# Kernel tuning notes

Hardware: AMD Instinct MI355X
Metric: run time of the kernel (lower is better)

The kernel has to match this reference:

```python
import jax, jax.numpy as jnp
import numpy as np

N_FFT = 2048
HOP = 441
DIM = 512


def _hann(n_fft):
    # torch.hann_window (periodic): 0.5*(1 - cos(2*pi*n/N))
    n = jnp.arange(n_fft, dtype=jnp.float32)
    return 0.5 * (1.0 - jnp.cos(2.0 * jnp.pi * n / n_fft))


def setup_inputs() -> dict:
    key = jax.random.key(0)
    k1, k2, k3 = jax.random.split(key, 3)
    x = jax.random.normal(k1, (4, 2, 1323000), dtype=jnp.float32)
    W_enc = 1e-4 * jax.random.normal(k2, (DIM, N_FFT), dtype=jnp.float32)
    W_dec = 1e-4 * jax.random.normal(k3, (N_FFT, DIM), dtype=jnp.float32)
    return {"x": x, "W_enc": W_enc, "W_dec": W_dec, "length": 1323000}


def reference(x, W_enc, W_dec, length):
    b, c, L = x.shape
    pad = N_FFT // 2
    window = _hann(N_FFT)

    # ---- encode ----
    xp = jnp.pad(x, ((0, 0), (0, 0), (pad, pad)), mode="reflect")  # (b,c,L+n_fft)
    Lp = xp.shape[-1]
    t = (Lp - N_FFT) // HOP + 1  # num frames
    idx = jnp.arange(t)[:, None] * HOP + jnp.arange(N_FFT)[None, :]  # (t, n)
    frames = xp[..., idx] * window  # (b,c,t,n) -- the overlapping unfold buffer
    feat = jnp.einsum("bctn,mn->bctm", frames, W_enc)  # (b,c,t,dim)

    # ---- decode ----
    rec = jnp.einsum("bctm,nm->bctn", feat, W_dec)  # (b,c,t,n)
    L2 = N_FFT + (t - 1) * HOP
    # overlap-add (F.fold) over merged (b*c) rows
    out = jnp.zeros((b * c, L2), dtype=rec.dtype)
    out = out.at[:, idx].add(rec.reshape(b * c, t, N_FFT))
    # window normalization (second fold in the original)
    win_norm = jnp.zeros((L2,), dtype=rec.dtype)
    win_norm = win_norm.at[idx].add(jnp.broadcast_to(window, (t, N_FFT)))
    out = out / jnp.clip(win_norm, 1e-8)
    out = out.reshape(b, c, L2)[..., pad:pad + length]
    return out
```

## Files before the change

### kernel.cpp

```cpp
#include <hip/hip_runtime.h>
#include <stdint.h>

typedef unsigned short u16;
typedef unsigned int u32;
typedef __attribute__((ext_vector_type(8))) short short8;
typedef __attribute__((ext_vector_type(4))) float f32x4;

#define L_IN   1323000
#define PAD    1024
#define HOP    441
#define T_FR   3001
#define M_ROWS 24008
#define NB     3008
#define RPAD   448
#define K1E    2240
#define K2     2560
#define W_2PI_N 3.0679615757712823e-3f

__device__ __forceinline__ u16 f2bf(float f) {
  union { float f; u32 u; } v; v.f = f;
  u32 r = v.u + 0x7FFFu + ((v.u >> 16) & 1u);
  return (u16)(r >> 16);
}

__device__ __forceinline__ void gload16(const void* g, void* l) {
  __builtin_amdgcn_global_load_lds(
      (const __attribute__((address_space(1))) u32*)g,
      (__attribute__((address_space(3))) u32*)l, 16, 0, 0);
}

__device__ __forceinline__ void tile_from_bid(int bid, int& m0, int& n0) {
  int g = (bid & 7) * 94 + (bid >> 3);
  m0 = (g >> 2) * 128;
  n0 = (g & 3) * 128;
}

__global__ void prep_all(const float* __restrict__ x,
                         const float* __restrict__ W_enc, const float* __restrict__ W_dec,
                         u16* __restrict__ xb, u16* __restrict__ wh2,
                         u16* __restrict__ b2, float* __restrict__ zeros) {
  int stride = gridDim.x * blockDim.x;
  int tid0 = blockIdx.x * blockDim.x + threadIdx.x;
  for (int idx = tid0; idx < 64; idx += stride) zeros[idx] = 0.f;
  for (int idx = tid0; idx < 8 * NB * RPAD; idx += stride) {
    int bc = idx / (NB * RPAD);
    int rem = idx - bc * (NB * RPAD);
    int u = rem / RPAD;
    int r = rem - u * RPAD;
    int s = HOP * u + r - PAD;
    int ja = s < 0 ? -s : s;
    int jb = 2 * L_IN - 2 - ja;
    int jr = ja < jb ? ja : jb;
    xb[idx] = f2bf(x[(size_t)bc * L_IN + jr]);
  }
  for (int idx = tid0; idx < 512 * K1E; idx += stride) {
    int m = idx / K1E;
    int k = idx - m * K1E;
    int j = k / RPAD;
    int r = k - j * RPAD;
    int n = HOP * j + r;
    float v = 0.f;
    if (r < HOP && n < 2048)
      v = (0.5f - 0.5f * cosf(W_2PI_N * (float)n)) * W_enc[m * 2048 + n];
    wh2[idx] = f2bf(v);
  }
  for (int idx = tid0; idx < 512 * K2; idx += stride) {
    int r = idx / K2;
    int k = idx - r * K2;
    int j = k >> 9;
    int m = k & 511;
    int n = HOP * j + r;
    float v = 0.f;
    if (r < HOP && n < 2048) {
      float s = 0.f;
      #pragma unroll
      for (int jj = 0; jj < 5; ++jj) {
        int nn = HOP * jj + r;
        if (nn < 2048) s += 0.5f - 0.5f * cosf(W_2PI_N * (float)nn);
      }
      v = W_dec[n * 512 + m] / fmaxf(s, 1e-8f);
    }
    b2[idx] = f2bf(v);
  }
}

__device__ __forceinline__ void mfma_tile(const u16* sA, const u16* sB, f32x4 acc[4][4],
                                          int lane, int wr, int wc) {
  const int lr = lane & 15;
  const int hi = lane >> 4;
  #pragma unroll
  for (int ks = 0; ks < 2; ++ks) {
    const int off = (((ks * 4 + hi) ^ (lr & 7)) << 3);
    short8 af[4], bg[4];
    #pragma unroll
    for (int f = 0; f < 4; ++f)
      af[f] = *(const short8*)(sA + (wr + f * 16 + lr) * 64 + off);
    #pragma unroll
    for (int f = 0; f < 4; ++f)
      bg[f] = *(const short8*)(sB + (wc + f * 16 + lr) * 64 + off);
    #pragma unroll
    for (int mf = 0; mf < 4; ++mf)
      #pragma unroll
      for (int nf = 0; nf < 4; ++nf)
        acc[mf][nf] = __builtin_amdgcn_mfma_f32_16x16x32_bf16(af[mf], bg[nf], acc[mf][nf], 0, 0, 0);
  }
}


__global__ __launch_bounds__(256, 2)
void gemm_enc(const u16* __restrict__ xb, const u16* __restrict__ wh2,
              u16* __restrict__ featb) {
  __shared__ u16 sA[128 * 64];
  __shared__ u16 sB[128 * 64];
  const int tid = threadIdx.x;
  const int lane = tid & 63;
  const int w = tid >> 6;
  int m0, n0;
  tile_from_bid(blockIdx.x, m0, n0);
  const int colsw = (((lane & 7) ^ ((lane >> 3) & 7)) << 3);

  const u16* bsrc[4];
  const u16* asrc[4];
  #pragma unroll
  for (int i = 0; i < 4; ++i) {
    int row = (i * 4 + w) * 8 + (lane >> 3);
    bsrc[i] = wh2 + (size_t)(n0 + row) * K1E + colsw;
    int rg = m0 + row;
    int rgc = rg < M_ROWS ? rg : (M_ROWS - 1);
    int bc = rgc / T_FR;
    int t  = rgc - bc * T_FR;
    asrc[i] = xb + ((size_t)bc * NB + t) * RPAD + colsw;
  }

  f32x4 acc[4][4];
  #pragma unroll
  for (int a = 0; a < 4; ++a)
    #pragma unroll
    for (int b = 0; b < 4; ++b) acc[a][b] = f32x4{0.f, 0.f, 0.f, 0.f};

  const int wr = (w >> 1) * 64, wc = (w & 1) * 64;

  for (int kc = 0; kc < K1E; kc += 64) {
    __syncthreads();
    #pragma unroll
    for (int i = 0; i < 4; ++i)
      gload16(bsrc[i] + kc, &sB[(i * 4 + w) * 512]);
    #pragma unroll
    for (int i = 0; i < 4; ++i)
      gload16(asrc[i] + kc, &sA[(i * 4 + w) * 512]);
    __syncthreads();
    mfma_tile(sA, sB, acc, lane, wr, wc);
  }

  #pragma unroll
  for (int mf = 0; mf < 4; ++mf) {
    #pragma unroll
    for (int e = 0; e < 4; ++e) {
      int rg = m0 + wr + mf * 16 + ((lane >> 4) << 2) + e;
      if (rg < M_ROWS) {
        #pragma unroll
        for (int nf = 0; nf < 4; ++nf) {
          int cg = n0 + wc + nf * 16 + (lane & 15);
          featb[(size_t)rg * 512 + cg] = f2bf(acc[mf][nf][e]);
        }
      }
    }
  }
}


__global__ __launch_bounds__(256, 2)
void gemm_dec(const u16* __restrict__ featb, const u16* __restrict__ b2,
              const u16* __restrict__ zeros, float* __restrict__ out) {
  __shared__ u16 sA[128 * 64];
  __shared__ u16 sB[128 * 64];
  const int tid = threadIdx.x;
  const int lane = tid & 63;
  const int w = tid >> 6;
  const int m0 = blockIdx.x * 128;
  const int n0 = blockIdx.y * 128;
  const int colsw = (((lane & 7) ^ ((lane >> 3) & 7)) << 3);

  const u16* bsrc[4];
  const u16* fsrc[4];
  int qiv[4];
  unsigned vmask = 0;
  #pragma unroll
  for (int i = 0; i < 4; ++i) {
    int row = (i * 4 + w) * 8 + (lane >> 3);
    bsrc[i] = b2 + (size_t)(n0 + row) * K2 + colsw;
    int rg = m0 + row;
    int rgc = rg < M_ROWS ? rg : (M_ROWS - 1);
    int bc = rgc / T_FR;
    int qi = rgc - bc * T_FR;
    if (rg < M_ROWS) vmask |= 1u << i;
    qiv[i] = qi;
    fsrc[i] = featb + (size_t)(bc * T_FR + qi + 2) * 512 + colsw;
  }

  f32x4 acc[4][4];
  #pragma unroll
  for (int a = 0; a < 4; ++a)
    #pragma unroll
    for (int b = 0; b < 4; ++b) acc[a][b] = f32x4{0.f, 0.f, 0.f, 0.f};

  const int wr = (w >> 1) * 64, wc = (w & 1) * 64;

  for (int kc = 0; kc < K2; kc += 64) {
    int jt = kc >> 9;
    __syncthreads();
    #pragma unroll
    for (int i = 0; i < 4; ++i)
      gload16(bsrc[i] + kc, &sB[(i * 4 + w) * 512]);
    #pragma unroll
    for (int i = 0; i < 4; ++i) {
      int t = qiv[i] + 2 - jt;
      bool ok = ((vmask >> i) & 1) && (t >= 0) && (t <= 3000);
      const u16* pa = ok ? (fsrc[i] + kc - 1024 * jt) : (zeros + colsw);
      gload16(pa, &sA[(i * 4 + w) * 512]);
    }
    __syncthreads();
    mfma_tile(sA, sB, acc, lane, wr, wc);
  }

  const int lr16 = lane & 15;
  #pragma unroll
  for (int mf = 0; mf < 4; ++mf) {
    #pragma unroll
    for (int e = 0; e < 4; ++e) {
      int rg = m0 + wr + mf * 16 + ((lane >> 4) << 2) + e;
      if (rg < M_ROWS) {
        int bc = rg / T_FR;
        int qi = rg - bc * T_FR;
        int ib = HOP * qi - 142;
        bool interior = (qi >= 2) && (qi <= 2998);
        #pragma unroll
        for (int nf = 0; nf < 4; ++nf) {
          int cg = n0 + wc + nf * 16 + lr16;
          if (cg < HOP) {
            int oi = ib + cg;
            if (oi >= 0 && oi < L_IN) {
              float v = acc[mf][nf][e];
              if (!interior) {
                float sf = 0.f, se = 0.f;
                #pragma unroll
                for (int j = 0; j < 5; ++j) {
                  int n = HOP * j + cg;
                  float h = (n < 2048) ? (0.5f - 0.5f * cosf(W_2PI_N * (float)n)) : 0.f;
                  sf += h;
                  if ((unsigned)(qi + 2 - j) <= 3000u) se += h;
                }
                v *= fmaxf(sf, 1e-8f) / fmaxf(se, 1e-8f);
              }
              out[(size_t)bc * L_IN + oi] = v;
            }
          }
        }
      }
    }
  }
}


extern "C" void kernel_launch(void* const* d_in, const int* in_sizes, int n_in,
                              void* d_out, int out_size, void* d_ws, size_t ws_size,
                              hipStream_t stream) {
  const float* x     = (const float*)d_in[0];
  const float* W_enc = (const float*)d_in[1];
  const float* W_dec = (const float*)d_in[2];
  float* out = (float*)d_out;
  char* ws = (char*)d_ws;

  u16* xb = (u16*)d_out;

  u16*   wh2   = (u16*)  (ws + 0);
  u16*   b2    = (u16*)  (ws + 2293760);
  u16*   featb = (u16*)  (ws + 4915200);
  float* zeros = (float*)(ws + 29499392);

  prep_all<<<2048, 256, 0, stream>>>(x, W_enc, W_dec, xb, wh2, b2, zeros);
  gemm_enc<<<752, 256, 0, stream>>>(xb, wh2, featb);
  gemm_dec<<<dim3(188, 4), 256, 0, stream>>>(featb, b2, (const u16*)zeros, out);
}
```

Baseline: 156.5 us.

## Precompose encoder and decoder weights into one convolution-like GEMM with edge fixup

Since encode and decode are both linear, the change composes W_dec and W_enc (with window and normalization folded in) into a single weight of shape 512x4032 over padded input samples. The main GEMM then maps raw framed input directly to output and no longer materializes the intermediate features. Edge frames, where the normalization differs, are handled by a tiny encoder GEMM, a dot-product kernel and a scatter. The main GEMM's K dimension grows from 2240+2560 to 4032 and the weight precomposition adds work. Composing the weights in bf16 and rounding the result back to bf16 changes numerical error.

```diff
diff --git a/kernel.cpp b/kernel.cpp
--- a/kernel.cpp
+++ b/kernel.cpp
@@ -11,10 +11,10 @@
 #define HOP    441
 #define T_FR   3001
 #define M_ROWS 24008
-#define NB     3008
+#define NBE    3016
 #define RPAD   448
 #define K1E    2240
-#define K2     2560
+#define KC     4032
 #define W_2PI_N 3.0679615757712823e-3f
 
 __device__ __forceinline__ u16 f2bf(float f) {
@@ -22,36 +22,36 @@
   u32 r = v.u + 0x7FFFu + ((v.u >> 16) & 1u);
   return (u16)(r >> 16);
 }
-
+__device__ __forceinline__ float bf2f(u16 s) {
+  union { u32 u; float f; } v; v.u = ((u32)s) << 16;
+  return v.f;
+}
 __device__ __forceinline__ void gload16(const void* g, void* l) {
   __builtin_amdgcn_global_load_lds(
       (const __attribute__((address_space(1))) u32*)g,
       (__attribute__((address_space(3))) u32*)l, 16, 0, 0);
 }
 
-__device__ __forceinline__ void tile_from_bid(int bid, int& m0, int& n0) {
-  int g = (bid & 7) * 94 + (bid >> 3);
-  m0 = (g >> 2) * 128;
-  n0 = (g & 3) * 128;
-}
-
 __global__ void prep_all(const float* __restrict__ x,
                          const float* __restrict__ W_enc, const float* __restrict__ W_dec,
-                         u16* __restrict__ xb, u16* __restrict__ wh2,
-                         u16* __restrict__ b2, float* __restrict__ zeros) {
+                         u16* __restrict__ xbe, u16* __restrict__ wh2,
+                         u16* __restrict__ wh2t, u16* __restrict__ b2) {
   int stride = gridDim.x * blockDim.x;
   int tid0 = blockIdx.x * blockDim.x + threadIdx.x;
-  for (int idx = tid0; idx < 64; idx += stride) zeros[idx] = 0.f;
-  for (int idx = tid0; idx < 8 * NB * RPAD; idx += stride) {
-    int bc = idx / (NB * RPAD);
-    int rem = idx - bc * (NB * RPAD);
+  for (int idx = tid0; idx < 8 * NBE * RPAD; idx += stride) {
+    int bc = idx / (NBE * RPAD);
+    int rem = idx - bc * (NBE * RPAD);
     int u = rem / RPAD;
     int r = rem - u * RPAD;
-    int s = HOP * u + r - PAD;
-    int ja = s < 0 ? -s : s;
-    int jb = 2 * L_IN - 2 - ja;
-    int jr = ja < jb ? ja : jb;
-    xb[idx] = f2bf(x[(size_t)bc * L_IN + jr]);
+    u16 v = 0;
+    if (u >= 4 && u <= 3008) {
+      int s = HOP * (u - 4) + r - PAD;
+      int ja = s < 0 ? -s : s;
+      int jb = 2 * L_IN - 2 - ja;
+      int jr = ja < jb ? ja : jb;
+      v = f2bf(x[(size_t)bc * L_IN + jr]);
+    }
+    xbe[idx] = v;
   }
   for (int idx = tid0; idx < 512 * K1E; idx += stride) {
     int m = idx / K1E;
@@ -62,11 +62,13 @@
     float v = 0.f;
     if (r < HOP && n < 2048)
       v = (0.5f - 0.5f * cosf(W_2PI_N * (float)n)) * W_enc[m * 2048 + n];
-    wh2[idx] = f2bf(v);
-  }
-  for (int idx = tid0; idx < 512 * K2; idx += stride) {
-    int r = idx / K2;
-    int k = idx - r * K2;
+    u16 b = f2bf(v);
+    wh2[idx] = b;
+    wh2t[k * 512 + m] = b;
+  }
+  for (int idx = tid0; idx < 512 * 2560; idx += stride) {
+    int r = idx / 2560;
+    int k = idx - r * 2560;
     int j = k >> 9;
     int m = k & 511;
     int n = HOP * j + r;
@@ -106,17 +108,89 @@
   }
 }
 
-
 __global__ __launch_bounds__(256, 2)
-void gemm_enc(const u16* __restrict__ xb, const u16* __restrict__ wh2,
-              u16* __restrict__ featb) {
+void ccomp_gemm(const u16* __restrict__ b2, const u16* __restrict__ wh2t,
+                u16* __restrict__ c_all) {
   __shared__ u16 sA[128 * 64];
   __shared__ u16 sB[128 * 64];
   const int tid = threadIdx.x;
   const int lane = tid & 63;
   const int w = tid >> 6;
-  int m0, n0;
-  tile_from_bid(blockIdx.x, m0, n0);
+  const int m0 = blockIdx.x * 128;
+  const int n0 = blockIdx.y * 128;
+  const int jj = blockIdx.z;
+  const int colsw = (((lane & 7) ^ ((lane >> 3) & 7)) << 3);
+
+  const u16* bsrc[4];
+  const u16* asrc[4];
+  #pragma unroll
+  for (int i = 0; i < 4; ++i) {
+    int row = (i * 4 + w) * 8 + (lane >> 3);
+    asrc[i] = b2 + (size_t)(m0 + row) * 2560 + 512 * jj + colsw;
+    int r2 = n0 + row; if (r2 > 2239) r2 = 2239;
+    bsrc[i] = wh2t + (size_t)r2 * 512 + colsw;
+  }
+
+  f32x4 acc[4][4];
+  #pragma unroll
+  for (int a = 0; a < 4; ++a)
+    #pragma unroll
+    for (int b = 0; b < 4; ++b) acc[a][b] = f32x4{0.f, 0.f, 0.f, 0.f};
+
+  const int wr = (w >> 1) * 64, wc = (w & 1) * 64;
+
+  for (int kc = 0; kc < 512; kc += 64) {
+    __syncthreads();
+    #pragma unroll
+    for (int i = 0; i < 4; ++i)
+      gload16(bsrc[i] + kc, &sB[(i * 4 + w) * 512]);
+    #pragma unroll
+    for (int i = 0; i < 4; ++i)
+      gload16(asrc[i] + kc, &sA[(i * 4 + w) * 512]);
+    __syncthreads();
+    mfma_tile(sA, sB, acc, lane, wr, wc);
+  }
+
+  #pragma unroll
+  for (int mf = 0; mf < 4; ++mf) {
+    #pragma unroll
+    for (int e = 0; e < 4; ++e) {
+      int rg = m0 + wr + mf * 16 + ((lane >> 4) << 2) + e;
+      #pragma unroll
+      for (int nf = 0; nf < 4; ++nf) {
+        int cg = n0 + wc + nf * 16 + (lane & 15);
+        if (cg < 2240)
+          c_all[(size_t)jj * 1146880 + (size_t)rg * 2240 + cg] = f2bf(acc[mf][nf][e]);
+      }
+    }
+  }
+}
+
+__global__ void ccfold(const u16* __restrict__ c_all, u16* __restrict__ ccomp) {
+  int stride = gridDim.x * blockDim.x;
+  for (int idx = blockIdx.x * blockDim.x + threadIdx.x; idx < 512 * KC; idx += stride) {
+    int r = idx / KC;
+    int u = idx - r * KC;
+    float s = 0.f;
+    #pragma unroll
+    for (int j = 0; j < 5; ++j) {
+      int k1 = u - (4 - j) * 448;
+      if (k1 >= 0 && k1 < K1E)
+        s += bf2f(c_all[(size_t)j * 1146880 + (size_t)r * 2240 + k1]);
+    }
+    ccomp[idx] = f2bf(s);
+  }
+}
+
+__global__ __launch_bounds__(256, 2)
+void enc_mini(const u16* __restrict__ xbe, const u16* __restrict__ wh2,
+              u16* __restrict__ featE) {
+  __shared__ u16 sA[128 * 64];
+  __shared__ u16 sB[128 * 64];
+  const int tid = threadIdx.x;
+  const int lane = tid & 63;
+  const int w = tid >> 6;
+  const int n0 = blockIdx.y * 128;
   const int colsw = (((lane & 7) ^ ((lane >> 3) & 7)) << 3);
 
   const u16* bsrc[4];
@@ -125,11 +199,11 @@
   for (int i = 0; i < 4; ++i) {
     int row = (i * 4 + w) * 8 + (lane >> 3);
     bsrc[i] = wh2 + (size_t)(n0 + row) * K1E + colsw;
-    int rg = m0 + row;
-    int rgc = rg < M_ROWS ? rg : (M_ROWS - 1);
-    int bc = rgc / T_FR;
-    int t  = rgc - bc * T_FR;
-    asrc[i] = xb + ((size_t)bc * NB + t) * RPAD + colsw;
+    int rgc = row < 64 ? row : 63;
+    int bci = rgc >> 3;
+    int f = rgc & 7;
+    int t = (f < 4) ? f : (2993 + f);
+    asrc[i] = xbe + (size_t)bci * (NBE * RPAD) + (size_t)(t + 4) * RPAD + colsw;
   }
 
   f32x4 acc[4][4];
@@ -156,22 +230,54 @@
   for (int mf = 0; mf < 4; ++mf) {
     #pragma unroll
     for (int e = 0; e < 4; ++e) {
-      int rg = m0 + wr + mf * 16 + ((lane >> 4) << 2) + e;
-      if (rg < M_ROWS) {
+      int rg = wr + mf * 16 + ((lane >> 4) << 2) + e;
+      if (rg < 64) {
         #pragma unroll
         for (int nf = 0; nf < 4; ++nf) {
           int cg = n0 + wc + nf * 16 + (lane & 15);
-          featb[(size_t)rg * 512 + cg] = f2bf(acc[mf][nf][e]);
+          featE[(size_t)rg * 512 + cg] = f2bf(acc[mf][nf][e]);
         }
       }
     }
   }
 }
 
+__global__ void edge2(const u16* __restrict__ featE, const u16* __restrict__ b2,
+                      float* __restrict__ edge_vals) {
+  int idx = blockIdx.x * blockDim.x + threadIdx.x;
+  if (idx >= 448 * 32) return;
+  int r = idx >> 5;
+  int row = idx & 31;
+  int bci = row >> 2, qe = row & 3;
+  int qi = (qe < 2) ? qe : (2997 + qe);
+  float acc = 0.f;
+  for (int j = 0; j < 5; ++j) {
+    int t = qi + 2 - j;
+    if (t >= 0 && t <= 3000) {
+      int f = (t < 4) ? t : (t - 2993);
+      const u16* bp = b2 + (size_t)r * 2560 + 512 * j;
+      const u16* fp = featE + (size_t)(bci * 8 + f) * 512;
+      float s = 0.f;
+      #pragma unroll 8
+      for (int m = 0; m < 512; ++m) s += bf2f(bp[m]) * bf2f(fp[m]);
+      acc += s;
+    }
+  }
+  float sf = 0.f, se = 0.f;
+  #pragma unroll
+  for (int j = 0; j < 5; ++j) {
+    int n = HOP * j + r;
+    float h = (r < HOP && n < 2048) ? (0.5f - 0.5f * cosf(W_2PI_N * (float)n)) : 0.f;
+    sf += h;
+    int t = qi + 2 - j;
+    if (t >= 0 && t <= 3000) se += h;
+  }
+  edge_vals[row * 448 + r] = (r < HOP) ? acc * sf / fmaxf(se, 1e-8f) : 0.f;
+}
 
 __global__ __launch_bounds__(256, 2)
-void gemm_dec(const u16* __restrict__ featb, const u16* __restrict__ b2,
-              const u16* __restrict__ zeros, float* __restrict__ out) {
+void gemm_main(const u16* __restrict__ xbe, const u16* __restrict__ ccomp,
+               float* __restrict__ out) {
   __shared__ u16 sA[128 * 64];
   __shared__ u16 sB[128 * 64];
   const int tid = threadIdx.x;
@@ -182,20 +288,16 @@
   const int colsw = (((lane & 7) ^ ((lane >> 3) & 7)) << 3);
 
   const u16* bsrc[4];
-  const u16* fsrc[4];
-  int qiv[4];
-  unsigned vmask = 0;
+  const u16* asrc[4];
   #pragma unroll
   for (int i = 0; i < 4; ++i) {
     int row = (i * 4 + w) * 8 + (lane >> 3);
-    bsrc[i] = b2 + (size_t)(n0 + row) * K2 + colsw;
+    bsrc[i] = ccomp + (size_t)(n0 + row) * KC + colsw;
     int rg = m0 + row;
     int rgc = rg < M_ROWS ? rg : (M_ROWS - 1);
     int bc = rgc / T_FR;
     int qi = rgc - bc * T_FR;
-    if (rg < M_ROWS) vmask |= 1u << i;
-    qiv[i] = qi;
-    fsrc[i] = featb + (size_t)(bc * T_FR + qi + 2) * 512 + colsw;
+    asrc[i] = xbe + (size_t)bc * (NBE * RPAD) + (size_t)(qi + 2) * RPAD + colsw;
   }
 
   f32x4 acc[4][4];
@@ -206,19 +308,14 @@
 
   const int wr = (w >> 1) * 64, wc = (w & 1) * 64;
 
-  for (int kc = 0; kc < K2; kc += 64) {
-    int jt = kc >> 9;
+  for (int kc = 0; kc < KC; kc += 64) {
     __syncthreads();
     #pragma unroll
     for (int i = 0; i < 4; ++i)
       gload16(bsrc[i] + kc, &sB[(i * 4 + w) * 512]);
     #pragma unroll
-    for (int i = 0; i < 4; ++i) {
-      int t = qiv[i] + 2 - jt;
-      bool ok = ((vmask >> i) & 1) && (t >= 0) && (t <= 3000);
-      const u16* pa = ok ? (fsrc[i] + kc - 1024 * jt) : (zeros + colsw);
-      gload16(pa, &sA[(i * 4 + w) * 512]);
-    }
+    for (int i = 0; i < 4; ++i)
+      gload16(asrc[i] + kc, &sA[(i * 4 + w) * 512]);
     __syncthreads();
     mfma_tile(sA, sB, acc, lane, wr, wc);
   }
@@ -232,33 +329,30 @@
       if (rg < M_ROWS) {
         int bc = rg / T_FR;
         int qi = rg - bc * T_FR;
-        int ib = HOP * qi - 142;
-        bool interior = (qi >= 2) && (qi <= 2998);
-        #pragma unroll
-        for (int nf = 0; nf < 4; ++nf) {
-          int cg = n0 + wc + nf * 16 + lr16;
-          if (cg < HOP) {
-            int oi = ib + cg;
-            if (oi >= 0 && oi < L_IN) {
-              float v = acc[mf][nf][e];
-              if (!interior) {
-                float sf = 0.f, se = 0.f;
-                #pragma unroll
-                for (int j = 0; j < 5; ++j) {
-                  int n = HOP * j + cg;
-                  float h = (n < 2048) ? (0.5f - 0.5f * cosf(W_2PI_N * (float)n)) : 0.f;
-                  sf += h;
-                  if ((unsigned)(qi + 2 - j) <= 3000u) se += h;
-                }
-                v *= fmaxf(sf, 1e-8f) / fmaxf(se, 1e-8f);
-              }
-              out[(size_t)bc * L_IN + oi] = v;
-            }
+        if (qi >= 2 && qi <= 2998) {
+          int ib = HOP * qi - 142;
+          #pragma unroll
+          for (int nf = 0; nf < 4; ++nf) {
+            int cg = n0 + wc + nf * 16 + lr16;
+            if (cg < HOP)
+              out[(size_t)bc * L_IN + ib + cg] = acc[mf][nf][e];
           }
         }
       }
     }
   }
+}
+
+__global__ void edge_scatter(const float* __restrict__ edge_vals, float* __restrict__ out) {
+  int idx = blockIdx.x * blockDim.x + threadIdx.x;
+  if (idx >= 32 * 441) return;
+  int row = idx / 441;
+  int r = idx - row * 441;
+  int bci = row >> 2, qe = row & 3;
+  int qi = (qe < 2) ? qe : (2997 + qe);
+  int oi = HOP * qi + r - 142;
+  if (oi >= 0 && oi < L_IN)
+    out[(size_t)bci * L_IN + oi] = edge_vals[row * 448 + r];
 }
 
 
@@ -270,15 +364,23 @@
   const float* W_dec = (const float*)d_in[2];
   float* out = (float*)d_out;
   char* ws = (char*)d_ws;
-
-  u16* xb = (u16*)d_out;
-
-  u16*   wh2   = (u16*)  (ws + 0);
-  u16*   b2    = (u16*)  (ws + 2293760);
-  u16*   featb = (u16*)  (ws + 4915200);
-  float* zeros = (float*)(ws + 29499392);
-
-  prep_all<<<2048, 256, 0, stream>>>(x, W_enc, W_dec, xb, wh2, b2, zeros);
-  gemm_enc<<<752, 256, 0, stream>>>(xb, wh2, featb);
-  gemm_dec<<<dim3(188, 4), 256, 0, stream>>>(featb, b2, (const u16*)zeros, out);
-}
+  char* dob = (char*)d_out;
+
+  u16*   xbe   = (u16*)  (ws + 0);
+  u16*   ccomp = (u16*)  (ws + 21618688);
+  u16*   featE = (u16*)  (ws + 25747456);
+  float* evals = (float*)(ws + 25812992);
+
+  u16* wh2t  = (u16*)(dob + 0);
+  u16* b2    = (u16*)(dob + 2293760);
+  u16* c_all = (u16*)(dob + 4915200);
+  u16* wh2   = (u16*)(dob + 16384000);
+
+  prep_all  <<<2048, 256, 0, stream>>>(x, W_enc, W_dec, xbe, wh2, wh2t, b2);
+  ccomp_gemm<<<dim3(4, 18, 5), 256, 0, stream>>>(b2, wh2t, c_all);
+  ccfold    <<<2048, 256, 0, stream>>>(c_all, ccomp);
+  enc_mini  <<<dim3(1, 4), 256, 0, stream>>>(xbe, wh2, featE);
+  edge2     <<<56, 256, 0, stream>>>(featE, b2, evals);
+  gemm_main <<<dim3(188, 4), 256, 0, stream>>>(xbe, ccomp, out);
+  edge_scatter<<<56, 256, 0, stream>>>(evals, out);
+}
```

Result: slower. 241.1 us (+54.0%).
